# Optimization experiments

Measured on AMD Instinct MI355X. Metric: run time of the kernel, lower is better.

The kernel has to match this reference:

```python
import jax, jax.numpy as jnp
import numpy as np

NUM_EXPERTS = 8
TOP_K = 2
CAPACITY_FACTOR = 1.25


def setup_inputs() -> dict:
    key = jax.random.key(0)
    ks = jax.random.split(key, 5)
    B, S, D, H, E = 4, 2048, 1024, 2048, NUM_EXPERTS
    scale = 0.02
    return {
        "x": jax.random.normal(ks[0], (B, S, D), dtype=jnp.float32),
        "gate_w": jax.random.normal(ks[1], (E, D), dtype=jnp.float32) * scale,
        "gate_proj_w": jax.random.normal(ks[2], (E, H, D), dtype=jnp.float32) * scale,
        "up_proj_w": jax.random.normal(ks[3], (E, H, D), dtype=jnp.float32) * scale,
        "down_proj_w": jax.random.normal(ks[4], (E, D, H), dtype=jnp.float32) * scale,
    }


def reference(x, gate_w, gate_proj_w, up_proj_w, down_proj_w):
    B, S, D = x.shape
    E, K = NUM_EXPERTS, TOP_K
    T = B * S
    xf = x.reshape(T, D)

    # Router: softmax over expert logits, then top-k (eval mode: no aux loss)
    logits = xf @ gate_w.T                      # (T, E)
    probs = jax.nn.softmax(logits, axis=-1)
    top_p, top_i = jax.lax.top_k(probs, K)      # (T, K)
    w = top_p / (jnp.sum(top_p, axis=-1, keepdims=True) + 1e-9)  # (T, K)

    # Capacity drop: per (k, expert), keep only the first `capacity` tokens
    # in token order (matches torch loop which truncates nonzero indices).
    capacity = int(CAPACITY_FACTOR * T / E)
    oh = jax.nn.one_hot(top_i, E, dtype=jnp.int32)        # (T, K, E)
    rank = jnp.cumsum(oh, axis=0) - 1                     # rank within (k, e)
    my_rank = jnp.sum(rank * oh, axis=-1)                 # (T, K)
    keep = (my_rank < capacity).astype(w.dtype)

    # Combined per-token per-expert weight (dropped tokens get 0)
    comb = jnp.einsum("tk,tke->te", w * keep, oh.astype(w.dtype))  # (T, E)

    # Per-expert dense SwiGLU; zero-weight tokens contribute nothing,
    # which matches the masked gather/scatter-add of the original.
    out = jnp.zeros_like(xf)
    for e in range(E):
        g = jax.nn.silu(xf @ gate_proj_w[e].T)   # (T, H)
        u = xf @ up_proj_w[e].T                  # (T, H)
        y = (g * u) @ down_proj_w[e].T           # (T, D)
        out = out + comb[:, e:e + 1] * y
    return out.reshape(B, S, D)
```

## Files before the change

### kernel.cpp

```cpp
#include <hip/hip_runtime.h>
#include <hip/hip_bf16.h>
#include <stdint.h>

#define T_TOK 8192
#define D_DIM 1024
#define H_DIM 2048
#define E_NUM 8
#define CAP   1280
#define CAP2  2560

#define BM 128
#define BN 128
#define BK 32

typedef __attribute__((ext_vector_type(8))) short short8;
typedef __attribute__((ext_vector_type(4))) float float4v;
typedef __attribute__((address_space(1))) const unsigned int gu32;
typedef __attribute__((address_space(3))) unsigned int lu32;

static __device__ __forceinline__ unsigned short f2bf(float f) {
    unsigned int u = __float_as_uint(f);
    unsigned int r = (u + 0x7FFFu + ((u >> 16) & 1u)) >> 16;
    return (unsigned short)r;
}

static __device__ __forceinline__ void store4bf(unsigned short* d, float4 v) {
    union { unsigned short u[4]; uint2 q; } pk;
    pk.u[0] = f2bf(v.x); pk.u[1] = f2bf(v.y);
    pk.u[2] = f2bf(v.z); pk.u[3] = f2bf(v.w);
    *(uint2*)d = pk.q;
}

__global__ __launch_bounds__(256) void convert_k(
    const float* __restrict__ src, unsigned short* __restrict__ dst, int n4) {
    const int i = blockIdx.x * 256 + threadIdx.x;
    if (i >= n4) return;
    store4bf(dst + (size_t)i * 4, ((const float4*)src)[i]);
}

__global__ __launch_bounds__(64) void router_k(
    const float* __restrict__ x, const float* __restrict__ gw,
    int* __restrict__ topi, float* __restrict__ topw) {
    const int t = blockIdx.x;
    const int lane = threadIdx.x;
    const float* xr = x + (size_t)t * D_DIM;

    float p[E_NUM];
#pragma unroll
    for (int e = 0; e < E_NUM; ++e) p[e] = 0.f;
#pragma unroll
    for (int c = 0; c < 4; ++c) {
        const int idx = c * 256 + lane * 4;
        const float4 xv = *(const float4*)(xr + idx);
#pragma unroll
        for (int e = 0; e < E_NUM; ++e) {
            const float4 gv = *(const float4*)(gw + e * D_DIM + idx);
            p[e] += xv.x * gv.x + xv.y * gv.y + xv.z * gv.z + xv.w * gv.w;
        }
    }
#pragma unroll
    for (int e = 0; e < E_NUM; ++e) {
        float v = p[e];
#pragma unroll
        for (int off = 32; off >= 1; off >>= 1) v += __shfl_xor(v, off);
        p[e] = v;
    }
    if (lane == 0) {
        float mx = p[0];
#pragma unroll
        for (int e = 1; e < E_NUM; ++e) mx = fmaxf(mx, p[e]);
        float pe[E_NUM]; float s = 0.f;
#pragma unroll
        for (int e = 0; e < E_NUM; ++e) { pe[e] = expf(p[e] - mx); s += pe[e]; }
        const float inv = 1.f / s;
        int i0 = 0;
#pragma unroll
        for (int e = 1; e < E_NUM; ++e) if (pe[e] > pe[i0]) i0 = e;
        int i1 = -1;
#pragma unroll
        for (int e = 0; e < E_NUM; ++e) {
            if (e == i0) continue;
            if (i1 < 0 || pe[e] > pe[i1]) i1 = e;
        }
        const float p0 = pe[i0] * inv, p1 = pe[i1] * inv;
        const float wn = 1.f / (p0 + p1 + 1e-9f);
        topi[t * 2 + 0] = i0; topi[t * 2 + 1] = i1;
        topw[t * 2 + 0] = p0 * wn; topw[t * 2 + 1] = p1 * wn;
    }
}

__global__ __launch_bounds__(1024) void assign_k(
    const int* __restrict__ topi, const float* __restrict__ topw,
    int* __restrict__ tok_list, float* __restrict__ w_list,
    int* __restrict__ n_tot) {
    __shared__ int kept[2][E_NUM];
    __shared__ int ntotL[E_NUM];
    const int tid = threadIdx.x;
    const int wid = tid >> 6, lane = tid & 63;
    const int k = wid >> 3, e = wid & 7;
    const uint64_t lt = (1ull << lane) - 1ull;

    int total = 0;
    for (int base = 0; base < T_TOK; base += 64) {
        const int idx = topi[(base + lane) * 2 + k];
        total += __popcll(__ballot(idx == e));
    }
    if (lane == 0) kept[k][e] = min(total, CAP);
    __syncthreads();
    if (tid < E_NUM) {
        ntotL[tid] = kept[0][tid] + kept[1][tid];
        n_tot[tid] = ntotL[tid];
    }
    const int myBase = e * CAP2 + (k ? kept[0][e] : 0);

    int running = 0, keptRun = 0;
    for (int base = 0; base < T_TOK; base += 64) {
        const int t = base + lane;
        const bool pred = (topi[t * 2 + k] == e);
        const uint64_t m = __ballot(pred);
        const int rank = running + __popcll(m & lt);
        const bool keep = pred && (rank < CAP);
        const uint64_t km = __ballot(keep);
        if (keep) {
            const int slot = myBase + keptRun + __popcll(km & lt);
            tok_list[slot] = t;
            w_list[slot] = topw[t * 2 + k];
        }
        running += __popcll(m);
        keptRun += __popcll(km);
    }
    __syncthreads();
    for (int s = tid; s < E_NUM * CAP2; s += 1024) {
        const int ee = s / CAP2, ls = s - ee * CAP2;
        if (ls >= ntotL[ee]) { tok_list[s] = 0; w_list[s] = 0.f; }
    }
}

__global__ __launch_bounds__(256, 2) void gateup_bf_k(
    const unsigned short* __restrict__ xbf,
    const unsigned short* __restrict__ wgbf, const unsigned short* __restrict__ wubf,
    const int* __restrict__ tok_list, const int* __restrict__ n_tot,
    unsigned short* __restrict__ h_ws, int e0) {
    const int ez = blockIdx.z;
    const int e = e0 + ez;
    const int m0 = blockIdx.y * BM;
    if (m0 >= n_tot[e]) return;
    const int n0 = blockIdx.x * BN;

    __shared__ __align__(1024) unsigned short smem[12288];

    const int tid = threadIdx.x, wid = tid >> 6, lane = tid & 63;

    const unsigned short* gsrc[6];
    int ldsoff[6];
#pragma unroll
    for (int i = 0; i < 6; ++i) {
        const int f = (wid * 6 + i) * 64 + lane;
        const unsigned short* g;
        if (f < 512) {
            const int row = f >> 2;
            const int tok = tok_list[e * CAP2 + m0 + row];
            g = xbf + (size_t)tok * D_DIM + (f & 3) * 8;
        } else if (f < 1024) {
            const int r = (f - 512) >> 2;
            g = wgbf + ((size_t)e * H_DIM + n0 + r) * D_DIM + (f & 3) * 8;
        } else {
            const int r = (f - 1024) >> 2;
            g = wubf + ((size_t)e * H_DIM + n0 + r) * D_DIM + (f & 3) * 8;
        }
        gsrc[i] = g;
        ldsoff[i] = (wid * 6 + i) * 1024;
    }

    float4v accg[4][4], accu[4][4];
#pragma unroll
    for (int i = 0; i < 4; ++i)
#pragma unroll
        for (int j = 0; j < 4; ++j) {
            accg[i][j] = (float4v){0.f, 0.f, 0.f, 0.f};
            accu[i][j] = (float4v){0.f, 0.f, 0.f, 0.f};
        }

    const int wm = (wid & 1) * 64, wn = (wid >> 1) * 64;
    const int frow = lane & 15;
    const int fk = (lane >> 4) * 8;

    for (int k0 = 0; k0 < D_DIM; k0 += BK) {
#pragma unroll
        for (int i = 0; i < 6; ++i)
            __builtin_amdgcn_global_load_lds(
                (gu32*)(gsrc[i] + k0),
                (lu32*)((char*)smem + ldsoff[i]), 16, 0, 0);
        __syncthreads();

        short8 af[4], bgf[4], buf[4];
#pragma unroll
        for (int i = 0; i < 4; ++i)
            af[i] = *(const short8*)&smem[(wm + i * 16 + frow) * 32 + fk];
#pragma unroll
        for (int j = 0; j < 4; ++j) {
            bgf[j] = *(const short8*)&smem[4096 + (wn + j * 16 + frow) * 32 + fk];
            buf[j] = *(const short8*)&smem[8192 + (wn + j * 16 + frow) * 32 + fk];
        }
#pragma unroll
        for (int i = 0; i < 4; ++i)
#pragma unroll
            for (int j = 0; j < 4; ++j) {
                accg[i][j] = __builtin_amdgcn_mfma_f32_16x16x32_bf16(af[i], bgf[j], accg[i][j], 0, 0, 0);
                accu[i][j] = __builtin_amdgcn_mfma_f32_16x16x32_bf16(af[i], buf[j], accu[i][j], 0, 0, 0);
            }
        __syncthreads();
    }

    const int col = lane & 15, rbase = (lane >> 4) * 4;
#pragma unroll
    for (int i = 0; i < 4; ++i)
#pragma unroll
        for (int j = 0; j < 4; ++j)
#pragma unroll
            for (int r = 0; r < 4; ++r) {
                const float g = accg[i][j][r];
                const float u = accu[i][j][r];
                const float hv = (g / (1.f + __expf(-g))) * u;
                const int m = wm + i * 16 + rbase + r;
                const int n = wn + j * 16 + col;
                h_ws[((size_t)ez * CAP2 + m0 + m) * H_DIM + (n0 + n)] = f2bf(hv);
            }
}

__global__ __launch_bounds__(256, 3) void down_bf_k(
    const unsigned short* __restrict__ h_ws, const unsigned short* __restrict__ wdbf,
    const int* __restrict__ tok_list, const float* __restrict__ w_list,
    const int* __restrict__ n_tot, float* __restrict__ out, int e0) {
    const int ez = blockIdx.z;
    const int e = e0 + ez;
    const int m0 = blockIdx.y * BM;
    if (m0 >= n_tot[e]) return;
    const int n0 = blockIdx.x * BN;

    __shared__ __align__(1024) unsigned short smem[8192];
    __shared__ int tokL[BM];
    __shared__ float wL[BM];

    const int tid = threadIdx.x, wid = tid >> 6, lane = tid & 63;
    if (tid < BM) {
        tokL[tid] = tok_list[e * CAP2 + m0 + tid];
        wL[tid] = w_list[e * CAP2 + m0 + tid];
    }

    const unsigned short* gsrc[4];
    int ldsoff[4];
#pragma unroll
    for (int i = 0; i < 4; ++i) {
        const int f = (wid * 4 + i) * 64 + lane;
        const unsigned short* g;
        if (f < 512) {
            const int row = f >> 2;
            g = h_ws + ((size_t)ez * CAP2 + m0 + row) * H_DIM + (f & 3) * 8;
        } else {
            const int r = (f - 512) >> 2;
            g = wdbf + ((size_t)e * D_DIM + n0 + r) * H_DIM + (f & 3) * 8;
        }
        gsrc[i] = g;
        ldsoff[i] = (wid * 4 + i) * 1024;
    }

    float4v acc[4][4];
#pragma unroll
    for (int i = 0; i < 4; ++i)
#pragma unroll
        for (int j = 0; j < 4; ++j) acc[i][j] = (float4v){0.f, 0.f, 0.f, 0.f};

    const int wm = (wid & 1) * 64, wn = (wid >> 1) * 64;
    const int frow = lane & 15;
    const int fk = (lane >> 4) * 8;

    for (int k0 = 0; k0 < H_DIM; k0 += BK) {
#pragma unroll
        for (int i = 0; i < 4; ++i)
            __builtin_amdgcn_global_load_lds(
                (gu32*)(gsrc[i] + k0),
                (lu32*)((char*)smem + ldsoff[i]), 16, 0, 0);
        __syncthreads();

        short8 af[4], bf[4];
#pragma unroll
        for (int i = 0; i < 4; ++i)
            af[i] = *(const short8*)&smem[(wm + i * 16 + frow) * 32 + fk];
#pragma unroll
        for (int j = 0; j < 4; ++j)
            bf[j] = *(const short8*)&smem[4096 + (wn + j * 16 + frow) * 32 + fk];
#pragma unroll
        for (int i = 0; i < 4; ++i)
#pragma unroll
            for (int j = 0; j < 4; ++j)
                acc[i][j] = __builtin_amdgcn_mfma_f32_16x16x32_bf16(af[i], bf[j], acc[i][j], 0, 0, 0);
        __syncthreads();
    }

    const int col = lane & 15, rbase = (lane >> 4) * 4;
#pragma unroll
    for (int i = 0; i < 4; ++i)
#pragma unroll
        for (int j = 0; j < 4; ++j)
#pragma unroll
            for (int r = 0; r < 4; ++r) {
                const int m = wm + i * 16 + rbase + r;
                const int n = wn + j * 16 + col;
                const float v = acc[i][j][r] * wL[m];
                unsafeAtomicAdd(&out[(size_t)tokL[m] * D_DIM + n0 + n], v);
            }
}

__global__ __launch_bounds__(256, 2) void gateup_legacy_k(
    const float* __restrict__ x,
    const float* __restrict__ wg_all, const float* __restrict__ wu_all,
    const int* __restrict__ tok_list, const int* __restrict__ n_tot,
    unsigned short* __restrict__ h_ws, int e0) {
    const int ez = blockIdx.z;
    const int e = e0 + ez;
    const int m0 = blockIdx.y * BM;
    if (m0 >= n_tot[e]) return;
    const int n0 = blockIdx.x * BN;

    __shared__ __align__(16) unsigned short As[BM][BK];
    __shared__ __align__(16) unsigned short Bg[BN][BK];
    __shared__ __align__(16) unsigned short Bu[BN][BK];
    __shared__ int tokL[BM];

    const int tid = threadIdx.x;
    if (tid < BM) tokL[tid] = tok_list[e * CAP2 + m0 + tid];
    __syncthreads();

    const float* wg = wg_all + (size_t)e * H_DIM * D_DIM;
    const float* wu = wu_all + (size_t)e * H_DIM * D_DIM;

    const float* aSrc[4]; const float* gSrc[4]; const float* uSrc[4];
    unsigned short* aDst[4]; unsigned short* gDst[4]; unsigned short* uDst[4];
#pragma unroll
    for (int it = 0; it < 4; ++it) {
        const int fid = it * 256 + tid;
        const int row = fid >> 3;
        const int c4 = (fid & 7) * 4;
        aSrc[it] = x + (size_t)tokL[row] * D_DIM + c4;
        gSrc[it] = wg + (size_t)(n0 + row) * D_DIM + c4;
        uSrc[it] = wu + (size_t)(n0 + row) * D_DIM + c4;
        aDst[it] = &As[row][c4];
        gDst[it] = &Bg[row][c4];
        uDst[it] = &Bu[row][c4];
    }

    float4v accg[4][4], accu[4][4];
#pragma unroll
    for (int i = 0; i < 4; ++i)
#pragma unroll
        for (int j = 0; j < 4; ++j) {
            accg[i][j] = (float4v){0.f, 0.f, 0.f, 0.f};
            accu[i][j] = (float4v){0.f, 0.f, 0.f, 0.f};
        }

    const int wid = tid >> 6, lane = tid & 63;
    const int wm = (wid & 1) * 64, wn = (wid >> 1) * 64;
    const int frow = lane & 15;
    const int fk = (lane >> 4) * 8;

    for (int k0 = 0; k0 < D_DIM; k0 += BK) {
#pragma unroll
        for (int it = 0; it < 4; ++it) {
            store4bf(aDst[it], *(const float4*)(aSrc[it] + k0));
            store4bf(gDst[it], *(const float4*)(gSrc[it] + k0));
            store4bf(uDst[it], *(const float4*)(uSrc[it] + k0));
        }
        __syncthreads();
        short8 af[4], bgf[4], buf[4];
#pragma unroll
        for (int i = 0; i < 4; ++i)
            af[i] = *(const short8*)&As[wm + i * 16 + frow][fk];
#pragma unroll
        for (int j = 0; j < 4; ++j) {
            bgf[j] = *(const short8*)&Bg[wn + j * 16 + frow][fk];
            buf[j] = *(const short8*)&Bu[wn + j * 16 + frow][fk];
        }
#pragma unroll
        for (int i = 0; i < 4; ++i)
#pragma unroll
            for (int j = 0; j < 4; ++j) {
                accg[i][j] = __builtin_amdgcn_mfma_f32_16x16x32_bf16(af[i], bgf[j], accg[i][j], 0, 0, 0);
                accu[i][j] = __builtin_amdgcn_mfma_f32_16x16x32_bf16(af[i], buf[j], accu[i][j], 0, 0, 0);
            }
        __syncthreads();
    }

    const int col = lane & 15, rbase = (lane >> 4) * 4;
#pragma unroll
    for (int i = 0; i < 4; ++i)
#pragma unroll
        for (int j = 0; j < 4; ++j)
#pragma unroll
            for (int r = 0; r < 4; ++r) {
                const float g = accg[i][j][r];
                const float u = accu[i][j][r];
                const float hv = (g / (1.f + __expf(-g))) * u;
                const int m = wm + i * 16 + rbase + r;
                const int n = wn + j * 16 + col;
                h_ws[((size_t)ez * CAP2 + m0 + m) * H_DIM + (n0 + n)] = f2bf(hv);
            }
}

__global__ __launch_bounds__(256, 2) void down_legacy_k(
    const unsigned short* __restrict__ h_ws, const float* __restrict__ wd_all,
    const int* __restrict__ tok_list, const float* __restrict__ w_list,
    const int* __restrict__ n_tot, float* __restrict__ out, int e0) {
    const int ez = blockIdx.z;
    const int e = e0 + ez;
    const int m0 = blockIdx.y * BM;
    if (m0 >= n_tot[e]) return;
    const int n0 = blockIdx.x * BN;

    __shared__ __align__(16) unsigned short As[BM][BK];
    __shared__ __align__(16) unsigned short Bs[BN][BK];
    __shared__ int tokL[BM];
    __shared__ float wL[BM];

    const int tid = threadIdx.x;
    if (tid < BM) {
        tokL[tid] = tok_list[e * CAP2 + m0 + tid];
        wL[tid] = w_list[e * CAP2 + m0 + tid];
    }
    __syncthreads();

    const unsigned short* hA = h_ws + ((size_t)ez * CAP2 + m0) * H_DIM;
    const float* wd = wd_all + (size_t)e * D_DIM * H_DIM;

    const unsigned short* aSrc[2]; unsigned short* aDst[2];
#pragma unroll
    for (int it = 0; it < 2; ++it) {
        const int fid = it * 256 + tid;
        const int row = fid >> 2;
        const int c8 = (fid & 3) * 8;
        aSrc[it] = hA + (size_t)row * H_DIM + c8;
        aDst[it] = &As[row][c8];
    }
    const float* bSrc[4]; unsigned short* bDst[4];
#pragma unroll
    for (int it = 0; it < 4; ++it) {
        const int fid = it * 256 + tid;
        const int row = fid >> 3;
        const int c4 = (fid & 7) * 4;
        bSrc[it] = wd + (size_t)(n0 + row) * H_DIM + c4;
        bDst[it] = &Bs[row][c4];
    }

    float4v acc[4][4];
#pragma unroll
    for (int i = 0; i < 4; ++i)
#pragma unroll
        for (int j = 0; j < 4; ++j) acc[i][j] = (float4v){0.f, 0.f, 0.f, 0.f};

    const int wid = tid >> 6, lane = tid & 63;
    const int wm = (wid & 1) * 64, wn = (wid >> 1) * 64;
    const int frow = lane & 15;
    const int fk = (lane >> 4) * 8;

    for (int k0 = 0; k0 < H_DIM; k0 += BK) {
#pragma unroll
        for (int it = 0; it < 2; ++it)
            *(uint4*)aDst[it] = *(const uint4*)(aSrc[it] + k0);
#pragma unroll
        for (int it = 0; it < 4; ++it)
            store4bf(bDst[it], *(const float4*)(bSrc[it] + k0));
        __syncthreads();
        short8 af[4], bf[4];
#pragma unroll
        for (int i = 0; i < 4; ++i)
            af[i] = *(const short8*)&As[wm + i * 16 + frow][fk];
#pragma unroll
        for (int j = 0; j < 4; ++j)
            bf[j] = *(const short8*)&Bs[wn + j * 16 + frow][fk];
#pragma unroll
        for (int i = 0; i < 4; ++i)
#pragma unroll
            for (int j = 0; j < 4; ++j)
                acc[i][j] = __builtin_amdgcn_mfma_f32_16x16x32_bf16(af[i], bf[j], acc[i][j], 0, 0, 0);
        __syncthreads();
    }

    const int col = lane & 15, rbase = (lane >> 4) * 4;
#pragma unroll
    for (int i = 0; i < 4; ++i)
#pragma unroll
        for (int j = 0; j < 4; ++j)
#pragma unroll
            for (int r = 0; r < 4; ++r) {
                const int m = wm + i * 16 + rbase + r;
                const int n = wn + j * 16 + col;
                const float v = acc[i][j][r] * wL[m];
                unsafeAtomicAdd(&out[(size_t)tokL[m] * D_DIM + n0 + n], v);
            }
}

extern "C" void kernel_launch(void* const* d_in, const int* in_sizes, int n_in,
                              void* d_out, int out_size, void* d_ws, size_t ws_size,
                              hipStream_t stream) {
    const float* x        = (const float*)d_in[0];
    const float* gate_w   = (const float*)d_in[1];
    const float* gate_pw  = (const float*)d_in[2];
    const float* up_pw    = (const float*)d_in[3];
    const float* down_pw  = (const float*)d_in[4];
    float* out = (float*)d_out;
    (void)n_in; (void)in_sizes; (void)out_size;

    uint8_t* ws = (uint8_t*)d_ws;
    size_t off = 0;
    int*   topi     = (int*)(ws + off);   off += (size_t)T_TOK * 2 * 4;
    float* topw     = (float*)(ws + off); off += (size_t)T_TOK * 2 * 4;
    int*   tok_list = (int*)(ws + off);   off += (size_t)E_NUM * CAP2 * 4;
    float* w_list   = (float*)(ws + off); off += (size_t)E_NUM * CAP2 * 4;
    int*   n_tot    = (int*)(ws + off);   off += 256;
    off = (off + 4095) & ~(size_t)4095;
    const size_t routing_end = off;

    const size_t x_elems = (size_t)T_TOK * D_DIM;
    const size_t w_elems = (size_t)E_NUM * H_DIM * D_DIM;
    unsigned short* xbf  = (unsigned short*)(ws + off); off += x_elems * 2;
    unsigned short* wgbf = (unsigned short*)(ws + off); off += w_elems * 2;
    unsigned short* wubf = (unsigned short*)(ws + off); off += w_elems * 2;
    unsigned short* wdbf = (unsigned short*)(ws + off); off += w_elems * 2;
    const size_t need_base = off;
    const size_t per_e = (size_t)CAP2 * H_DIM * 2;

    hipMemsetAsync(out, 0, (size_t)T_TOK * D_DIM * sizeof(float), stream);
    router_k<<<T_TOK, 64, 0, stream>>>(x, gate_w, topi, topw);
    assign_k<<<1, 1024, 0, stream>>>(topi, topw, tok_list, w_list, n_tot);

    if (ws_size >= need_base + per_e) {
        unsigned short* h_ws = (unsigned short*)(ws + need_base);
        int chunk = (int)((ws_size - need_base) / per_e);
        if (chunk > E_NUM) chunk = E_NUM;

        const int w4 = (int)(w_elems / 4), x4 = (int)(x_elems / 4);
        convert_k<<<(w4 + 255) / 256, 256, 0, stream>>>(gate_pw, wgbf, w4);
        convert_k<<<(w4 + 255) / 256, 256, 0, stream>>>(up_pw, wubf, w4);
        convert_k<<<(w4 + 255) / 256, 256, 0, stream>>>(down_pw, wdbf, w4);
        convert_k<<<(x4 + 255) / 256, 256, 0, stream>>>(x, xbf, x4);

        for (int e0 = 0; e0 < E_NUM; e0 += chunk) {
            const int ne = (e0 + chunk <= E_NUM) ? chunk : (E_NUM - e0);
            dim3 g1(H_DIM / BN, CAP2 / BM, ne);
            gateup_bf_k<<<g1, 256, 0, stream>>>(xbf, wgbf, wubf, tok_list, n_tot, h_ws, e0);
            dim3 g2(D_DIM / BN, CAP2 / BM, ne);
            down_bf_k<<<g2, 256, 0, stream>>>(h_ws, wdbf, tok_list, w_list, n_tot, out, e0);
        }
    } else {
        unsigned short* h_ws = (unsigned short*)(ws + routing_end);
        int chunk = (ws_size > routing_end) ? (int)((ws_size - routing_end) / per_e) : 0;
        if (chunk > E_NUM) chunk = E_NUM;
        if (chunk < 1) chunk = 1;

        for (int e0 = 0; e0 < E_NUM; e0 += chunk) {
            const int ne = (e0 + chunk <= E_NUM) ? chunk : (E_NUM - e0);
            dim3 g1(H_DIM / BN, CAP2 / BM, ne);
            gateup_legacy_k<<<g1, 256, 0, stream>>>(x, gate_pw, up_pw, tok_list, n_tot, h_ws, e0);
            dim3 g2(D_DIM / BN, CAP2 / BM, ne);
            down_legacy_k<<<g2, 256, 0, stream>>>(h_ws, down_pw, tok_list, w_list, n_tot, out, e0);
        }
    }
}
```

Baseline: 715.4 us.

## Fuse conversions, batch router tokens, stage topi in LDS, deepen down-proj K tile

New measurement: 671.8 us. -6.1%, faster.

```diff
diff --git a/kernel.cpp b/kernel.cpp
--- a/kernel.cpp
+++ b/kernel.cpp
@@ -31,18 +31,30 @@
     *(uint2*)d = pk.q;
 }
 
-__global__ __launch_bounds__(256) void convert_k(
-    const float* __restrict__ src, unsigned short* __restrict__ dst, int n4) {
-    const int i = blockIdx.x * 256 + threadIdx.x;
-    if (i >= n4) return;
-    store4bf(dst + (size_t)i * 4, ((const float4*)src)[i]);
-}
-
-__global__ __launch_bounds__(64) void router_k(
+__global__ __launch_bounds__(256) void convert_all_k(
+    const float* __restrict__ wg, const float* __restrict__ wu,
+    const float* __restrict__ wd, const float* __restrict__ x,
+    unsigned short* __restrict__ wgbf, unsigned short* __restrict__ wubf,
+    unsigned short* __restrict__ wdbf, unsigned short* __restrict__ xbf) {
+    const int W4 = E_NUM * H_DIM * D_DIM / 4;
+    const int X4 = T_TOK * D_DIM / 4;
+    const int total = 3 * W4 + X4;
+    const int stride = gridDim.x * 256;
+    for (int i = blockIdx.x * 256 + threadIdx.x; i < total; i += stride) {
+        const float* s; unsigned short* d; int j;
+        if (i < W4)            { s = wg; d = wgbf; j = i; }
+        else if (i < 2 * W4)   { s = wu; d = wubf; j = i - W4; }
+        else if (i < 3 * W4)   { s = wd; d = wdbf; j = i - 2 * W4; }
+        else                   { s = x;  d = xbf;  j = i - 3 * W4; }
+        store4bf(d + (size_t)j * 4, ((const float4*)s)[j]);
+    }
+}
+
+__global__ __launch_bounds__(256) void router_k(
     const float* __restrict__ x, const float* __restrict__ gw,
     int* __restrict__ topi, float* __restrict__ topw) {
-    const int t = blockIdx.x;
-    const int lane = threadIdx.x;
+    const int t = blockIdx.x * 4 + (threadIdx.x >> 6);
+    const int lane = threadIdx.x & 63;
     const float* xr = x + (size_t)t * D_DIM;
 
     float p[E_NUM];
@@ -93,6 +105,7 @@
     const int* __restrict__ topi, const float* __restrict__ topw,
     int* __restrict__ tok_list, float* __restrict__ w_list,
     int* __restrict__ n_tot) {
+    __shared__ unsigned char topiL[T_TOK * 2];
     __shared__ int kept[2][E_NUM];
     __shared__ int ntotL[E_NUM];
     const int tid = threadIdx.x;
@@ -100,9 +113,18 @@
     const int k = wid >> 3, e = wid & 7;
     const uint64_t lt = (1ull << lane) - 1ull;
 
+    for (int i = tid; i < T_TOK * 2 / 4; i += 1024) {
+        const int4 v = ((const int4*)topi)[i];
+        uchar4 b;
+        b.x = (unsigned char)v.x; b.y = (unsigned char)v.y;
+        b.z = (unsigned char)v.z; b.w = (unsigned char)v.w;
+        ((uchar4*)topiL)[i] = b;
+    }
+    __syncthreads();
+
     int total = 0;
     for (int base = 0; base < T_TOK; base += 64) {
-        const int idx = topi[(base + lane) * 2 + k];
+        const int idx = topiL[(base + lane) * 2 + k];
         total += __popcll(__ballot(idx == e));
     }
     if (lane == 0) kept[k][e] = min(total, CAP);
@@ -116,7 +138,7 @@
     int running = 0, keptRun = 0;
     for (int base = 0; base < T_TOK; base += 64) {
         const int t = base + lane;
-        const bool pred = (topi[t * 2 + k] == e);
+        const bool pred = (topiL[t * 2 + k] == e);
         const uint64_t m = __ballot(pred);
         const int rank = running + __popcll(m & lt);
         const bool keep = pred && (rank < CAP);
@@ -228,7 +250,7 @@
             }
 }
 
-__global__ __launch_bounds__(256, 3) void down_bf_k(
+__global__ __launch_bounds__(256, 2) void down_bf_k(
     const unsigned short* __restrict__ h_ws, const unsigned short* __restrict__ wdbf,
     const int* __restrict__ tok_list, const float* __restrict__ w_list,
     const int* __restrict__ n_tot, float* __restrict__ out, int e0) {
@@ -238,7 +260,7 @@
     if (m0 >= n_tot[e]) return;
     const int n0 = blockIdx.x * BN;
 
-    __shared__ __align__(1024) unsigned short smem[8192];
+    __shared__ __align__(1024) unsigned short smem[16384];
     __shared__ int tokL[BM];
     __shared__ float wL[BM];
 
@@ -248,21 +270,22 @@
         wL[tid] = w_list[e * CAP2 + m0 + tid];
     }
 
-    const unsigned short* gsrc[4];
-    int ldsoff[4];
-#pragma unroll
-    for (int i = 0; i < 4; ++i) {
-        const int f = (wid * 4 + i) * 64 + lane;
+    const unsigned short* gsrc[8];
+    int ldsoff[8];
+#pragma unroll
+    for (int i = 0; i < 8; ++i) {
+        const int f = (wid * 8 + i) * 64 + lane;
         const unsigned short* g;
-        if (f < 512) {
-            const int row = f >> 2;
-            g = h_ws + ((size_t)ez * CAP2 + m0 + row) * H_DIM + (f & 3) * 8;
+        if (f < 1024) {
+            const int r = f >> 3, c = (f & 7) ^ (r & 7);
+            g = h_ws + ((size_t)ez * CAP2 + m0 + r) * H_DIM + c * 8;
         } else {
-            const int r = (f - 512) >> 2;
-            g = wdbf + ((size_t)e * D_DIM + n0 + r) * H_DIM + (f & 3) * 8;
+            const int fr = f - 1024;
+            const int r = fr >> 3, c = (fr & 7) ^ (r & 7);
+            g = wdbf + ((size_t)e * D_DIM + n0 + r) * H_DIM + c * 8;
         }
         gsrc[i] = g;
-        ldsoff[i] = (wid * 4 + i) * 1024;
+        ldsoff[i] = (wid * 8 + i) * 1024;
     }
 
     float4v acc[4][4];
@@ -273,28 +296,38 @@
 
     const int wm = (wid & 1) * 64, wn = (wid >> 1) * 64;
     const int frow = lane & 15;
-    const int fk = (lane >> 4) * 8;
-
-    for (int k0 = 0; k0 < H_DIM; k0 += BK) {
-#pragma unroll
-        for (int i = 0; i < 4; ++i)
+    const int quad = lane >> 4;
+
+    for (int k0 = 0; k0 < H_DIM; k0 += 64) {
+#pragma unroll
+        for (int i = 0; i < 8; ++i)
             __builtin_amdgcn_global_load_lds(
                 (gu32*)(gsrc[i] + k0),
                 (lu32*)((char*)smem + ldsoff[i]), 16, 0, 0);
         __syncthreads();
 
-        short8 af[4], bf[4];
-#pragma unroll
-        for (int i = 0; i < 4; ++i)
-            af[i] = *(const short8*)&smem[(wm + i * 16 + frow) * 32 + fk];
-#pragma unroll
-        for (int j = 0; j < 4; ++j)
-            bf[j] = *(const short8*)&smem[4096 + (wn + j * 16 + frow) * 32 + fk];
-#pragma unroll
-        for (int i = 0; i < 4; ++i)
-#pragma unroll
-            for (int j = 0; j < 4; ++j)
-                acc[i][j] = __builtin_amdgcn_mfma_f32_16x16x32_bf16(af[i], bf[j], acc[i][j], 0, 0, 0);
+        short8 af[2][4], bf[2][4];
+#pragma unroll
+        for (int s = 0; s < 2; ++s) {
+            const int c = s * 4 + quad;
+#pragma unroll
+            for (int i = 0; i < 4; ++i) {
+                const int row = wm + i * 16 + frow;
+                af[s][i] = *(const short8*)&smem[(row * 8 + (c ^ (row & 7))) * 8];
+            }
+#pragma unroll
+            for (int j = 0; j < 4; ++j) {
+                const int row = wn + j * 16 + frow;
+                bf[s][j] = *(const short8*)&smem[8192 + (row * 8 + (c ^ (row & 7))) * 8];
+            }
+        }
+#pragma unroll
+        for (int s = 0; s < 2; ++s)
+#pragma unroll
+            for (int i = 0; i < 4; ++i)
+#pragma unroll
+                for (int j = 0; j < 4; ++j)
+                    acc[i][j] = __builtin_amdgcn_mfma_f32_16x16x32_bf16(af[s][i], bf[s][j], acc[i][j], 0, 0, 0);
         __syncthreads();
     }
 
@@ -530,7 +563,7 @@
     const size_t per_e = (size_t)CAP2 * H_DIM * 2;
 
     hipMemsetAsync(out, 0, (size_t)T_TOK * D_DIM * sizeof(float), stream);
-    router_k<<<T_TOK, 64, 0, stream>>>(x, gate_w, topi, topw);
+    router_k<<<T_TOK / 4, 256, 0, stream>>>(x, gate_w, topi, topw);
     assign_k<<<1, 1024, 0, stream>>>(topi, topw, tok_list, w_list, n_tot);
 
     if (ws_size >= need_base + per_e) {
@@ -538,11 +571,8 @@
         int chunk = (int)((ws_size - need_base) / per_e);
         if (chunk > E_NUM) chunk = E_NUM;
 
-        const int w4 = (int)(w_elems / 4), x4 = (int)(x_elems / 4);
-        convert_k<<<(w4 + 255) / 256, 256, 0, stream>>>(gate_pw, wgbf, w4);
-        convert_k<<<(w4 + 255) / 256, 256, 0, stream>>>(up_pw, wubf, w4);
-        convert_k<<<(w4 + 255) / 256, 256, 0, stream>>>(down_pw, wdbf, w4);
-        convert_k<<<(x4 + 255) / 256, 256, 0, stream>>>(x, xbf, x4);
+        convert_all_k<<<4096, 256, 0, stream>>>(gate_pw, up_pw, down_pw, x,
+                                                wgbf, wubf, wdbf, xbf);
 
         for (int e0 = 0; e0 < E_NUM; e0 += chunk) {
             const int ne = (e0 + chunk <= E_NUM) ? chunk : (E_NUM - e0);
```
